# Optimization experiments

Measured on AMD Instinct MI355X. Metric: run time of the kernel, lower is better.

Reference implementation:

```python
import jax, jax.numpy as jnp
import numpy as np

B, C_IN, M = 512, 200, 128  # M = n_nodes + 1 (zero-pad slot 0)
N3 = 3 * (M - 1)            # 3 gather indices (node,left,right) per node
H1, H2, F = 512, 512, 256   # conv channel sizes, F = feature_dim


def tree_conv(data, idx, w, b):
    # data: [B, C, M]; idx: [B, 3N] int indices into M; w: [O, C, 3]; b: [O]
    gathered = jnp.take_along_axis(data, idx[:, None, :].astype(jnp.int32), axis=2)  # [B, C, 3N]
    g = gathered.reshape(data.shape[0], data.shape[1], -1, 3)  # [B, C, N, 3]
    out = jnp.einsum('bcnk,ock->bon', g, w) + b[None, :, None]  # Conv1d(k=3, stride=3)
    zero = jnp.zeros((data.shape[0], w.shape[0], 1), out.dtype)  # re-attach pad slot 0
    return jnp.concatenate([zero, out], axis=2)  # [B, O, M]


def tree_layer_norm(data):
    # per-tree normalization over (channel, node) dims; torch.std is unbiased (ddof=1)
    mean = jnp.mean(data, axis=(1, 2), keepdims=True)
    std = jnp.std(data, axis=(1, 2), keepdims=True, ddof=1)
    return (data - mean) / (std + 1e-5)


def setup_inputs() -> dict:
    key = jax.random.key(0)
    ks = jax.random.split(key, 16)
    s = 0.05
    inp = {
        'trees': jax.random.normal(ks[0], (B, C_IN, M), jnp.float32),
        'indexes': jax.random.randint(ks[1], (B, N3, 1), 0, M, jnp.int32),
        # plan_embedding_nn conv stack
        'w1': jax.random.normal(ks[2], (H1, C_IN, 3), jnp.float32) * s,
        'b1': jnp.zeros((H1,), jnp.float32),
        'w2': jax.random.normal(ks[3], (H2, H1, 3), jnp.float32) * s,
        'b2': jnp.zeros((H2,), jnp.float32),
        'w3': jax.random.normal(ks[4], (F, H2, 3), jnp.float32) * s,
        'b3': jnp.zeros((F,), jnp.float32),
        # gate_nn: Linear(F, F//2) ReLU Linear(F//2, 1)
        'gw1': jax.random.normal(ks[5], (F // 2, F), jnp.float32) * s,
        'gb1': jnp.zeros((F // 2,), jnp.float32),
        'gw2': jax.random.normal(ks[6], (1, F // 2), jnp.float32) * s,
        'gb2': jnp.zeros((1,), jnp.float32),
        'rw1': jax.random.normal(ks[7], (128, 2 * F), jnp.float32) * s,
        'rb1': jnp.zeros((128,), jnp.float32),
        'rw2': jax.random.normal(ks[8], (64, 128), jnp.float32) * s,
        'rb2': jnp.zeros((64,), jnp.float32),
        'rw3': jax.random.normal(ks[9], (1, 64), jnp.float32) * s,
        'rb3': jnp.zeros((1,), jnp.float32),
    }
    return inp


def reference(trees, indexes, w1, b1, w2, b2, w3, b3, gw1, gb1, gw2, gb2,
              rw1, rb1, rw2, rb2, rw3, rb3):
    idx = indexes[..., 0]  # [B, 3N]
    x = jax.nn.relu(tree_layer_norm(tree_conv(trees, idx, w1, b1)))
    x = jax.nn.relu(tree_layer_norm(tree_conv(x, idx, w2, b2)))
    emb = tree_conv(x, idx, w3, b3)            # [B, F, M]
    et = jnp.transpose(emb, (0, 2, 1))         # [B, M, F]
    # GlobalAttention pooling: segments are the equal-size per-plan node sets,
    # so segment-softmax == softmax over the node axis.
    gate = jax.nn.relu(jnp.einsum('bmf,hf->bmh', et, gw1) + gb1)
    gate = jnp.einsum('bmh,oh->bmo', gate, gw2) + gb2   # [B, M, 1]
    attn = jax.nn.softmax(gate, axis=1)
    pool = jnp.sum(attn * et, axis=1)          # [B, F]
    root = et[:, 1, :]                         # slot 1 = root node
    combined = jnp.concatenate([root, pool], axis=1)  # [B, 2F]
    h = jax.nn.relu(combined @ rw1.T + rb1)
    h = jax.nn.relu(h @ rw2.T + rb2)
    out = h @ rw3.T + rb3                      # [B, 1]
    return out, combined
```

## Files before the change

### kernel.cpp

```cpp
#include <hip/hip_runtime.h>
#include <stdint.h>

#define DI __device__ __forceinline__

static constexpr int B_   = 512;
static constexpr int N3_  = 381;

typedef short bf16x8 __attribute__((ext_vector_type(8)));
typedef float f32x4  __attribute__((ext_vector_type(4)));

DI float bf2f(uint32_t u) { union { uint32_t i; float f; } v; v.i = u << 16; return v.f; }
DI uint16_t f2bf(float f) {
  union { float f; uint32_t i; } v; v.f = f;
  uint32_t x = v.i;
  return (uint16_t)((x + 0x7fffu + ((x >> 16) & 1u)) >> 16);
}
DI void unpack8(uint4 u, float* v) {
  v[0] = bf2f(u.x & 0xffffu); v[1] = bf2f(u.x >> 16);
  v[2] = bf2f(u.y & 0xffffu); v[3] = bf2f(u.y >> 16);
  v[4] = bf2f(u.z & 0xffffu); v[5] = bf2f(u.z >> 16);
  v[6] = bf2f(u.w & 0xffffu); v[7] = bf2f(u.w >> 16);
}

DI void ldsload16(const uint16_t* g, uint16_t* l) {
  __builtin_amdgcn_global_load_lds((const __attribute__((address_space(1))) void*)g,
                                   (__attribute__((address_space(3))) void*)l,
                                   16, 0, 0);
}

__global__ void probe_kernel(const uint16_t* __restrict__ trees, int* __restrict__ flag,
                             float* __restrict__ statsAcc) {
  __shared__ int cnt;
  if (threadIdx.x == 0) cnt = 0;
  __syncthreads();
  int local = 0;
  #pragma unroll
  for (int q = 0; q < 2; q++) {
    uint16_t u = trees[threadIdx.x * 2 + q];
    int ex = (u >> 7) & 0xff;
    if (ex >= 110 && ex <= 133) local++;
  }
  atomicAdd(&cnt, local);
  #pragma unroll
  for (int q = 0; q < 8; q++) statsAcc[q * 256 + threadIdx.x] = 0.f;
  __syncthreads();
  if (threadIdx.x == 0) *flag = (cnt >= 450) ? 0 : 1;
}

__global__ void cvt_to_bf16(const void* __restrict__ src, uint16_t* __restrict__ dst,
                            int n, const int* __restrict__ flag) {
  int isf32 = *flag;
  int stride = gridDim.x * blockDim.x;
  for (int i = blockIdx.x * blockDim.x + threadIdx.x; i < n; i += stride)
    dst[i] = isf32 ? f2bf(((const float*)src)[i]) : ((const uint16_t*)src)[i];
}

__global__ void wcvt_kernel(const void* __restrict__ src, uint16_t* __restrict__ dst,
                            int O, int C, int Cpad, const int* __restrict__ flag) {
  int isf32 = *flag;
  int Kpad = 3 * Cpad;
  int n = O * Kpad;
  int stride = gridDim.x * blockDim.x;
  for (int i = blockIdx.x * blockDim.x + threadIdx.x; i < n; i += stride) {
    int o = i / Kpad, e = i - o * Kpad;
    int reg = e / Cpad, c = e - reg * Cpad;
    uint16_t v = 0;
    if (c < C) {
      int s = (o * C + c) * 3 + reg;
      v = isf32 ? f2bf(((const float*)src)[s]) : ((const uint16_t*)src)[s];
    }
    dst[i] = v;
  }
}

struct CvtJob { const void* src; float* dst; int n; };
struct CvtJobs { CvtJob j[13]; };
__global__ void cvt_many(CvtJobs jobs, int nj, const int* __restrict__ flag) {
  int isf32 = *flag;
  int stride = gridDim.x * blockDim.x;
  for (int k = 0; k < nj; k++) {
    const void* src = jobs.j[k].src;
    float* dst = jobs.j[k].dst;
    int n = jobs.j[k].n;
    for (int i = blockIdx.x * blockDim.x + threadIdx.x; i < n; i += stride)
      dst[i] = isf32 ? ((const float*)src)[i] : bf2f(((const uint16_t*)src)[i]);
  }
}

__global__ __launch_bounds__(256)
void transpose_trees(const void* __restrict__ trees, uint16_t* __restrict__ dst,
                     const int* __restrict__ flag) {
  __shared__ uint16_t sX[32][130];
  const int b = blockIdx.y, c0 = blockIdx.x * 32, tx = threadIdx.x;
  const int cn = min(32, 200 - c0);
  const int isf32 = *flag;

  if (isf32) {
    const float* src = (const float*)trees + ((size_t)b * 200 + c0) * 128;
    for (int t = tx; t < cn * 128; t += 256) {
      int c = t >> 7, m = t & 127;
      sX[c][m] = f2bf(src[c * 128 + m]);
    }
  } else {
    const uint32_t* src = (const uint32_t*)((const uint16_t*)trees + ((size_t)b * 200 + c0) * 128);
    for (int t = tx; t < cn * 64; t += 256) {
      int c = t >> 6, p = t & 63;
      ((uint32_t*)&sX[c][0])[p] = src[c * 64 + p];
    }
  }
  __syncthreads();

  uint32_t* out = (uint32_t*)(dst + (size_t)b * 129 * 256 + c0);
  for (int p = tx; p < 129 * 16; p += 256) {
    int m = p >> 4, u = p & 15;
    int c = u * 2;
    uint32_t v = 0;
    if (m < 128) {
      uint16_t lo = (c     < cn) ? sX[c][m]     : (uint16_t)0;
      uint16_t hi = (c + 1 < cn) ? sX[c + 1][m] : (uint16_t)0;
      v = (uint32_t)lo | ((uint32_t)hi << 16);
    }
    out[(size_t)m * 128 + u] = v;
  }
}

__global__ __launch_bounds__(256, 3)
void gemm_kernel(const uint16_t* __restrict__ A,
                 const uint16_t* __restrict__ xT,
                 const int* __restrict__ idxg,
                 const float* __restrict__ bias,
                 uint16_t* __restrict__ Y,
                 int nO, int Cpad, int outRS,
                 float* __restrict__ statsAcc) {
  __shared__ __align__(16) uint16_t sA[128 * 64];
  __shared__ __align__(16) uint16_t sB[128 * 64];
  __shared__ float sBias[128];
  __shared__ int sIdx[384];
  __shared__ float2 sRed[256];

  const int id   = blockIdx.x;
  const int xcd  = id & 7;
  const int rest = id >> 3;
  const int ot   = rest % nO;
  const int b    = (rest / nO) * 8 + xcd;
  const int obase = ot * 128;
  const int O     = nO * 128;

  const int tx    = threadIdx.x;
  const int wave  = tx >> 6, lane = tx & 63;
  const int wj    = wave & 1, wo = wave >> 1;
  const int Kpad  = 3 * Cpad;

  for (int t = tx; t < N3_; t += 256) sIdx[t] = idxg[(size_t)b * N3_ + t];
  if (tx < 128) sBias[tx] = bias[obase + tx];
  __syncthreads();

  const uint16_t* Abase = A + (size_t)obase * Kpad;
  const uint16_t* Bbase = xT + (size_t)b * 129 * Cpad;

  const int srow = lane >> 3;
  const int schk = lane & 7;
  const int lm = lane & 15;
  const int kg = lane >> 4;

  f32x4 zero4 = {0.f, 0.f, 0.f, 0.f};
  f32x4 acc[4][4];
  #pragma unroll
  for (int i = 0; i < 4; i++)
    #pragma unroll
    for (int j = 0; j < 4; j++) acc[i][j] = zero4;

  for (int reg = 0; reg < 3; reg++) {
    int ridx[4];
    #pragma unroll
    for (int i = 0; i < 4; i++) {
      int r = wave * 8 + i * 32 + srow;
      ridx[i] = (r == 0) ? 128 : sIdx[3 * (r - 1) + reg];
    }
    for (int co = 0; co < Cpad; co += 64) {
      __syncthreads();
      #pragma unroll
      for (int i = 0; i < 4; i++) {
        int r  = wave * 8 + i * 32 + srow;
        int ca = schk ^ (r & 7);
        ldsload16(Abase + (size_t)r * Kpad + reg * Cpad + co + ca * 8,
                  &sA[(wave * 8 + i * 32) * 64]);
        ldsload16(Bbase + (size_t)ridx[i] * Cpad + co + ca * 8,
                  &sB[(wave * 8 + i * 32) * 64]);
      }
      __syncthreads();
      #pragma unroll
      for (int s = 0; s < 2; s++) {
        bf16x8 xv[4], wv[4];
        #pragma unroll
        for (int f = 0; f < 4; f++) {
          int rj = wj * 64 + f * 16 + lm;
          int cj = (s * 4 + kg) ^ (rj & 7);
          xv[f] = *(const bf16x8*)&sB[rj * 64 + cj * 8];
          int ro = wo * 64 + f * 16 + lm;
          int cw = (s * 4 + kg) ^ (ro & 7);
          wv[f] = *(const bf16x8*)&sA[ro * 64 + cw * 8];
        }
        #pragma unroll
        for (int fj = 0; fj < 4; fj++)
          #pragma unroll
          for (int fo = 0; fo < 4; fo++)
            acc[fj][fo] = __builtin_amdgcn_mfma_f32_16x16x32_bf16(xv[fj], wv[fo], acc[fj][fo], 0, 0, 0);
      }
    }
  }

  float s1 = 0.f, s2 = 0.f;
  #pragma unroll
  for (int fj = 0; fj < 4; fj++) {
    #pragma unroll
    for (int fo = 0; fo < 4; fo++) {
      int olocal = wo * 64 + fo * 16 + lm;
      float bo = sBias[olocal];
      #pragma unroll
      for (int r = 0; r < 4; r++) {
        int j = wj * 64 + fj * 16 + kg * 4 + r;
        float v = acc[fj][fo][r] + bo;
        if (j == 0) v = 0.f;
        s1 += v; s2 += v * v;
        Y[((size_t)b * outRS + j) * O + obase + olocal] = f2bf(v);
      }
    }
  }

  if (statsAcc) {
    sRed[tx] = make_float2(s1, s2);
    __syncthreads();
    for (int s = 128; s > 0; s >>= 1) {
      if (tx < s) { sRed[tx].x += sRed[tx + s].x; sRed[tx].y += sRed[tx + s].y; }
      __syncthreads();
    }
    if (tx == 0) {
      atomicAdd(&statsAcc[b * 2],     sRed[0].x);
      atomicAdd(&statsAcc[b * 2 + 1], sRed[0].y);
    }
  }
}

__global__ void stats_finalize(const float* __restrict__ acc, float* __restrict__ ms,
                               int count, int nb) {
  int b = blockIdx.x * blockDim.x + threadIdx.x;
  if (b < nb) {
    float s = acc[b * 2], ss = acc[b * 2 + 1];
    float n = (float)count;
    float mean = s / n;
    float var = (ss - s * s / n) / (n - 1.0f);
    var = fmaxf(var, 0.f);
    ms[b * 2] = mean;
    ms[b * 2 + 1] = 1.0f / (sqrtf(var) + 1e-5f);
  }
}

__global__ __launch_bounds__(256)
void ln_relu_kernel(uint16_t* __restrict__ y, const float* __restrict__ ms) {
  const int total = B_ * 129 * 64;
  int stride = gridDim.x * blockDim.x;
  for (int i = blockIdx.x * blockDim.x + threadIdx.x; i < total; i += stride) {
    int rowG = i >> 6;
    int b = rowG / 129;
    int r = rowG - b * 129;
    uint4 out;
    if (r == 128) {
      out = make_uint4(0, 0, 0, 0);
    } else {
      float mean = ms[b * 2], scale = ms[b * 2 + 1];
      uint4 u = ((const uint4*)y)[i];
      float v[8]; unpack8(u, v);
      uint32_t rr[4];
      #pragma unroll
      for (int k = 0; k < 4; k++) {
        float a  = fmaxf((v[2 * k]     - mean) * scale, 0.f);
        float bb = fmaxf((v[2 * k + 1] - mean) * scale, 0.f);
        rr[k] = (uint32_t)f2bf(a) | ((uint32_t)f2bf(bb) << 16);
      }
      out = make_uint4(rr[0], rr[1], rr[2], rr[3]);
    }
    ((uint4*)y)[i] = out;
  }
}

__global__ __launch_bounds__(256)
void gate_kernel(const uint16_t* __restrict__ emb,
                 const uint16_t* __restrict__ gw1b,
                 const float* __restrict__ gb1,
                 const float* __restrict__ gw2, const float* __restrict__ gb2,
                 const float* __restrict__ rw1, const float* __restrict__ rb1,
                 const float* __restrict__ rw2, const float* __restrict__ rb2,
                 const float* __restrict__ rw3, const float* __restrict__ rb3,
                 void* __restrict__ dout, const int* __restrict__ flag) {
  __shared__ __align__(16) uint16_t sEmb[128 * 64];
  __shared__ float sRed[4][128];
  __shared__ float sSm[128];
  __shared__ float sAttn[128];
  __shared__ float sPool4[4 * 256];
  __shared__ __align__(16) float sC[512];
  __shared__ __align__(16) float sH1[128];
  __shared__ float sH2[64];

  const int b = blockIdx.x;
  const int tx = threadIdx.x;
  const int wave = tx >> 6, lane = tx & 63;
  const int lm = lane & 15, kg = lane >> 4;
  const int srow = lane >> 3, schk = lane & 7;
  const int h0 = wave * 32;
  const uint16_t* embB = emb + (size_t)b * 128 * 256;

  f32x4 zero4 = {0.f, 0.f, 0.f, 0.f};
  f32x4 acc[2][8];
  #pragma unroll
  for (int i = 0; i < 2; i++)
    #pragma unroll
    for (int t = 0; t < 8; t++) acc[i][t] = zero4;

  for (int kc = 0; kc < 256; kc += 64) {
    __syncthreads();
    #pragma unroll
    for (int i = 0; i < 4; i++) {
      int r  = wave * 8 + i * 32 + srow;
      int ca = schk ^ (r & 7);
      ldsload16(embB + (size_t)r * 256 + kc + ca * 8, &sEmb[(wave * 8 + i * 32) * 64]);
    }
    __syncthreads();
    #pragma unroll
    for (int s = 0; s < 2; s++) {
      bf16x8 a0 = *(const bf16x8*)(gw1b + (size_t)(h0 + lm) * 256 + kc + s * 32 + kg * 8);
      bf16x8 a1 = *(const bf16x8*)(gw1b + (size_t)(h0 + 16 + lm) * 256 + kc + s * 32 + kg * 8);
      #pragma unroll
      for (int t = 0; t < 8; t++) {
        int rn = t * 16 + lm;
        int cn = (s * 4 + kg) ^ (rn & 7);
        bf16x8 bv = *(const bf16x8*)&sEmb[rn * 64 + cn * 8];
        acc[0][t] = __builtin_amdgcn_mfma_f32_16x16x32_bf16(a0, bv, acc[0][t], 0, 0, 0);
        acc[1][t] = __builtin_amdgcn_mfma_f32_16x16x32_bf16(a1, bv, acc[1][t], 0, 0, 0);
      }
    }
  }

  float gb[2][4], gv[2][4];
  #pragma unroll
  for (int ht = 0; ht < 2; ht++)
    #pragma unroll
    for (int r = 0; r < 4; r++) {
      int h = h0 + ht * 16 + kg * 4 + r;
      gb[ht][r] = gb1[h]; gv[ht][r] = gw2[h];
    }
  float p[8];
  #pragma unroll
  for (int t = 0; t < 8; t++) {
    float s = 0.f;
    #pragma unroll
    for (int ht = 0; ht < 2; ht++)
      #pragma unroll
      for (int r = 0; r < 4; r++)
        s += fmaxf(acc[ht][t][r] + gb[ht][r], 0.f) * gv[ht][r];
    s += __shfl_xor(s, 16);
    s += __shfl_xor(s, 32);
    p[t] = s;
  }
  if (lane < 16) {
    #pragma unroll
    for (int t = 0; t < 8; t++) sRed[wave][t * 16 + lane] = p[t];
  }
  __syncthreads();

  float e = 0.f;
  if (tx < 128) {
    float v = sRed[0][tx] + sRed[1][tx] + sRed[2][tx] + sRed[3][tx] + gb2[0];
    sSm[tx] = v;
    sAttn[tx] = v;
  }
  __syncthreads();
  for (int s = 64; s > 0; s >>= 1) {
    if (tx < s) sSm[tx] = fmaxf(sSm[tx], sSm[tx + s]);
    __syncthreads();
  }
  float mx = sSm[0];
  __syncthreads();
  if (tx < 128) { e = expf(sAttn[tx] - mx); sSm[tx] = e; }
  __syncthreads();
  for (int s = 64; s > 0; s >>= 1) {
    if (tx < s) sSm[tx] += sSm[tx + s];
    __syncthreads();
  }
  float denom = sSm[0];
  __syncthreads();
  if (tx < 128) sAttn[tx] = e / denom;
  __syncthreads();

  float pl00 = 0.f, pl01 = 0.f, pl10 = 0.f, pl11 = 0.f;
  const uint32_t* base = (const uint32_t*)embB;
  const int mw = wave * 32;
  for (int mi = 0; mi < 32; mi++) {
    float a = sAttn[mw + mi];
    uint32_t u0 = base[(size_t)(mw + mi) * 128 + lane];
    uint32_t u1 = base[(size_t)(mw + mi) * 128 + 64 + lane];
    pl00 = fmaf(a, bf2f(u0 & 0xffffu), pl00);
    pl01 = fmaf(a, bf2f(u0 >> 16),     pl01);
    pl10 = fmaf(a, bf2f(u1 & 0xffffu), pl10);
    pl11 = fmaf(a, bf2f(u1 >> 16),     pl11);
  }
  sPool4[wave * 256 + lane * 2]           = pl00;
  sPool4[wave * 256 + lane * 2 + 1]       = pl01;
  sPool4[wave * 256 + 128 + lane * 2]     = pl10;
  sPool4[wave * 256 + 128 + lane * 2 + 1] = pl11;
  __syncthreads();

  float pool = sPool4[tx] + sPool4[256 + tx] + sPool4[512 + tx] + sPool4[768 + tx];
  float root = bf2f(embB[256 + tx]);
  sC[tx]       = root;
  sC[256 + tx] = pool;

  const int isf32 = (*flag != 0);
  if (!isf32) {
    uint16_t* o = ((uint16_t*)dout) + 512;
    o[b * 512 + tx]       = f2bf(root);
    o[b * 512 + 256 + tx] = f2bf(pool);
  } else {
    float* o = ((float*)dout) + 512;
    o[b * 512 + tx]       = root;
    o[b * 512 + 256 + tx] = pool;
  }
  __syncthreads();

  if (tx < 128) {
    float a = rb1[tx];
    const float4* wr = (const float4*)(rw1 + (size_t)tx * 512);
    for (int i = 0; i < 128; i++) {
      float4 w4 = wr[i];
      float4 c4 = *(const float4*)&sC[i * 4];
      a = fmaf(w4.x, c4.x, a); a = fmaf(w4.y, c4.y, a);
      a = fmaf(w4.z, c4.z, a); a = fmaf(w4.w, c4.w, a);
    }
    sH1[tx] = fmaxf(a, 0.f);
  }
  __syncthreads();
  if (tx < 64) {
    float a2 = rb2[tx];
    const float4* wr2 = (const float4*)(rw2 + (size_t)tx * 128);
    for (int i = 0; i < 32; i++) {
      float4 w4 = wr2[i];
      float4 h4 = *(const float4*)&sH1[i * 4];
      a2 = fmaf(w4.x, h4.x, a2); a2 = fmaf(w4.y, h4.y, a2);
      a2 = fmaf(w4.z, h4.z, a2); a2 = fmaf(w4.w, h4.w, a2);
    }
    sH2[tx] = fmaxf(a2, 0.f);
  }
  __syncthreads();
  if (tx < 64) {
    float pv = sH2[tx] * rw3[tx];
    for (int off = 32; off > 0; off >>= 1) pv += __shfl_down(pv, off);
    if (tx == 0) {
      float o = pv + rb3[0];
      if (!isf32) ((uint16_t*)dout)[b] = f2bf(o);
      else        ((float*)dout)[b]    = o;
    }
  }
}

extern "C" void kernel_launch(void* const* d_in, const int* in_sizes, int n_in,
                              void* d_out, int out_size, void* d_ws, size_t ws_size,
                              hipStream_t stream) {
  const void* trees   = d_in[0];
  const int*  indexes = (const int*)d_in[1];
  const void* w1 = d_in[2];  const void* b1 = d_in[3];
  const void* w2 = d_in[4];  const void* b2 = d_in[5];
  const void* w3 = d_in[6];  const void* b3 = d_in[7];
  const void* gw1 = d_in[8]; const void* gb1 = d_in[9];
  const void* gw2 = d_in[10]; const void* gb2 = d_in[11];
  const void* rw1 = d_in[12]; const void* rb1 = d_in[13];
  const void* rw2 = d_in[14]; const void* rb2 = d_in[15];
  const void* rw3 = d_in[16]; const void* rb3 = d_in[17];

  char* ws = (char*)d_ws;
  size_t off = 0;
  auto alloc = [&](size_t bytes) -> char* {
    char* p = ws + off;
    off += (bytes + 255) & ~(size_t)255;
    return p;
  };

  int*   flagp    = (int*)alloc(256);
  float* statsAcc = (float*)alloc(4 * B_ * sizeof(float));
  float* statsMS  = (float*)alloc(4 * B_ * sizeof(float));
  float* b1f = (float*)alloc(512 * 4);
  float* b2f = (float*)alloc(512 * 4);
  float* b3f = (float*)alloc(256 * 4);
  float* gb1f = (float*)alloc(128 * 4);
  float* gw2f = (float*)alloc(128 * 4);
  float* gb2f = (float*)alloc(4);
  float* rw1f = (float*)alloc(128 * 512 * 4);
  float* rb1f = (float*)alloc(128 * 4);
  float* rw2f = (float*)alloc(64 * 128 * 4);
  float* rb2f = (float*)alloc(64 * 4);
  float* rw3f = (float*)alloc(64 * 4);
  float* rb3f = (float*)alloc(4);
  uint16_t* W1b  = (uint16_t*)alloc((size_t)512 * 768 * 2);
  uint16_t* W2b  = (uint16_t*)alloc((size_t)512 * 1536 * 2);
  uint16_t* W3b  = (uint16_t*)alloc((size_t)256 * 1536 * 2);
  uint16_t* GW1b = (uint16_t*)alloc((size_t)128 * 256 * 2);
  uint16_t* bufA = (uint16_t*)alloc((size_t)B_ * 129 * 512 * 2);
  uint16_t* bufB = (uint16_t*)alloc((size_t)B_ * 129 * 512 * 2);

  uint16_t* treesT = bufB;
  uint16_t* y1T    = bufA;
  uint16_t* y2T    = bufB;
  uint16_t* yT3    = bufA;

  probe_kernel<<<1, 256, 0, stream>>>((const uint16_t*)trees, flagp, statsAcc);
  transpose_trees<<<dim3(7, B_), 256, 0, stream>>>(trees, treesT, flagp);
  wcvt_kernel<<<1024, 256, 0, stream>>>(w1, W1b, 512, 200, 256, flagp);
  wcvt_kernel<<<2048, 256, 0, stream>>>(w2, W2b, 512, 512, 512, flagp);
  wcvt_kernel<<<1024, 256, 0, stream>>>(w3, W3b, 256, 512, 512, flagp);
  cvt_to_bf16<<<256, 256, 0, stream>>>(gw1, GW1b, 128 * 256, flagp);

  CvtJobs jobs;
  int ji = 0;
  auto addjob = [&](const void* s, float* d, int n) { jobs.j[ji].src = s; jobs.j[ji].dst = d; jobs.j[ji].n = n; ji++; };
  addjob(b1, b1f, 512); addjob(b2, b2f, 512); addjob(b3, b3f, 256);
  addjob(gb1, gb1f, 128);
  addjob(gw2, gw2f, 128);       addjob(gb2, gb2f, 1);
  addjob(rw1, rw1f, 128 * 512); addjob(rb1, rb1f, 128);
  addjob(rw2, rw2f, 64 * 128);  addjob(rb2, rb2f, 64);
  addjob(rw3, rw3f, 64);        addjob(rb3, rb3f, 1);
  cvt_many<<<256, 256, 0, stream>>>(jobs, ji, flagp);

  gemm_kernel<<<4 * B_, 256, 0, stream>>>(
      W1b, treesT, indexes, b1f, y1T, 4, 256, 129, statsAcc);
  stats_finalize<<<2, 256, 0, stream>>>(statsAcc, statsMS, 512 * 128, B_);
  ln_relu_kernel<<<2048, 256, 0, stream>>>(y1T, statsMS);

  gemm_kernel<<<4 * B_, 256, 0, stream>>>(
      W2b, y1T, indexes, b2f, y2T, 4, 512, 129, statsAcc + 2 * B_);
  stats_finalize<<<2, 256, 0, stream>>>(statsAcc + 2 * B_, statsMS + 2 * B_, 512 * 128, B_);
  ln_relu_kernel<<<2048, 256, 0, stream>>>(y2T, statsMS + 2 * B_);

  gemm_kernel<<<2 * B_, 256, 0, stream>>>(
      W3b, y2T, indexes, b3f, yT3, 2, 512, 128, nullptr);

  gate_kernel<<<B_, 256, 0, stream>>>(yT3, GW1b, gb1f, gw2f, gb2f,
                                      rw1f, rb1f, rw2f, rb2f, rw3f, rb3f,
                                      d_out, flagp);

  (void)in_sizes; (void)n_in; (void)out_size; (void)ws_size;
}
```

Baseline: 465.5 us.

## Merge preprocessing kernels into one launch and fold stats finalize into LN

Replaces the probe, transpose, weight-convert and small-parameter convert kernels with a single prep kernel that partitions its blocks by job, with every block recomputing the dtype probe locally. Removes the two stats_finalize launches by computing mean and inverse std inline in ln_relu_kernel. Also raises gemm_kernel launch bounds occupancy hint from 3 to 4. The aim is to cut launch count and inter-kernel gaps, at the cost of redundant probe work per block and possible register pressure in the GEMM.

```diff
diff --git a/kernel.cpp b/kernel.cpp
--- a/kernel.cpp
+++ b/kernel.cpp
@@ -28,40 +28,31 @@
                                    16, 0, 0);
 }
 
-__global__ void probe_kernel(const uint16_t* __restrict__ trees, int* __restrict__ flag,
-                             float* __restrict__ statsAcc) {
-  __shared__ int cnt;
-  if (threadIdx.x == 0) cnt = 0;
-  __syncthreads();
-  int local = 0;
-  #pragma unroll
-  for (int q = 0; q < 2; q++) {
-    uint16_t u = trees[threadIdx.x * 2 + q];
-    int ex = (u >> 7) & 0xff;
-    if (ex >= 110 && ex <= 133) local++;
-  }
-  atomicAdd(&cnt, local);
-  #pragma unroll
-  for (int q = 0; q < 8; q++) statsAcc[q * 256 + threadIdx.x] = 0.f;
-  __syncthreads();
-  if (threadIdx.x == 0) *flag = (cnt >= 450) ? 0 : 1;
-}
-
-__global__ void cvt_to_bf16(const void* __restrict__ src, uint16_t* __restrict__ dst,
-                            int n, const int* __restrict__ flag) {
-  int isf32 = *flag;
-  int stride = gridDim.x * blockDim.x;
-  for (int i = blockIdx.x * blockDim.x + threadIdx.x; i < n; i += stride)
-    dst[i] = isf32 ? f2bf(((const float*)src)[i]) : ((const uint16_t*)src)[i];
-}
-
-__global__ void wcvt_kernel(const void* __restrict__ src, uint16_t* __restrict__ dst,
-                            int O, int C, int Cpad, const int* __restrict__ flag) {
-  int isf32 = *flag;
+struct PrepArgs {
+  const void* trees; const void* w1; const void* w2; const void* w3; const void* gw1;
+  const void* b1; const void* b2; const void* b3; const void* gb1;
+  const void* gw2; const void* gb2;
+  const void* rw1; const void* rb1; const void* rw2; const void* rb2;
+  const void* rw3; const void* rb3;
+  uint16_t* treesT; uint16_t* W1b; uint16_t* W2b; uint16_t* W3b; uint16_t* GW1b;
+  float* b1f; float* b2f; float* b3f; float* gb1f; float* gw2f; float* gb2f;
+  float* rw1f; float* rb1f; float* rw2f; float* rb2f; float* rw3f; float* rb3f;
+  int* flagp; float* statsAcc;
+};
+
+static constexpr int PREP_TRANS_END = 3584;
+static constexpr int PREP_W1_END    = 3840;
+static constexpr int PREP_W2_END    = 4352;
+static constexpr int PREP_W3_END    = 4608;
+static constexpr int PREP_GW1_END   = 4640;
+static constexpr int PREP_F32_END   = 4672;
+  
+DI void wcvt_range(const void* src, uint16_t* dst, int O, int C, int Cpad,
+                   int isf32, int idx, int nb) {
   int Kpad = 3 * Cpad;
   int n = O * Kpad;
-  int stride = gridDim.x * blockDim.x;
-  for (int i = blockIdx.x * blockDim.x + threadIdx.x; i < n; i += stride) {
+  int stride = nb * 256;
+  for (int i = idx * 256 + (int)threadIdx.x; i < n; i += stride) {
     int o = i / Kpad, e = i - o * Kpad;
     int reg = e / Cpad, c = e - reg * Cpad;
     uint16_t v = 0;
@@ -73,58 +64,102 @@
   }
 }
 
-struct CvtJob { const void* src; float* dst; int n; };
-struct CvtJobs { CvtJob j[13]; };
-__global__ void cvt_many(CvtJobs jobs, int nj, const int* __restrict__ flag) {
-  int isf32 = *flag;
-  int stride = gridDim.x * blockDim.x;
-  for (int k = 0; k < nj; k++) {
-    const void* src = jobs.j[k].src;
-    float* dst = jobs.j[k].dst;
-    int n = jobs.j[k].n;
-    for (int i = blockIdx.x * blockDim.x + threadIdx.x; i < n; i += stride)
-      dst[i] = isf32 ? ((const float*)src)[i] : bf2f(((const uint16_t*)src)[i]);
-  }
+DI void fcvt_range(const void* src, float* dst, int n, int isf32, int idx, int nb) {
+  int stride = nb * 256;
+  for (int i = idx * 256 + (int)threadIdx.x; i < n; i += stride)
+    dst[i] = isf32 ? ((const float*)src)[i] : bf2f(((const uint16_t*)src)[i]);
 }
 
 __global__ __launch_bounds__(256)
-void transpose_trees(const void* __restrict__ trees, uint16_t* __restrict__ dst,
-                     const int* __restrict__ flag) {
+void prep_kernel(PrepArgs a) {
+  __shared__ int cnt;
   __shared__ uint16_t sX[32][130];
-  const int b = blockIdx.y, c0 = blockIdx.x * 32, tx = threadIdx.x;
-  const int cn = min(32, 200 - c0);
-  const int isf32 = *flag;
-
-  if (isf32) {
-    const float* src = (const float*)trees + ((size_t)b * 200 + c0) * 128;
-    for (int t = tx; t < cn * 128; t += 256) {
-      int c = t >> 7, m = t & 127;
-      sX[c][m] = f2bf(src[c * 128 + m]);
-    }
+
+  const int id = blockIdx.x;
+  const int tx = threadIdx.x;
+
+  if (tx == 0) cnt = 0;
+  __syncthreads();
+  {
+    const uint16_t* t16 = (const uint16_t*)a.trees;
+    int local = 0;
+    #pragma unroll
+    for (int q = 0; q < 2; q++) {
+      uint16_t u = t16[tx * 2 + q];
+      int ex = (u >> 7) & 0xff;
+      if (ex >= 110 && ex <= 133) local++;
+    }
+    atomicAdd(&cnt, local);
+  }
+  __syncthreads();
+  const int isf32 = (cnt >= 450) ? 0 : 1;
+
+  if (id == 0) {
+    if (tx == 0) *a.flagp = isf32;
+    #pragma unroll
+    for (int q = 0; q < 8; q++) a.statsAcc[q * 256 + tx] = 0.f;
+  }
+
+  if (id < PREP_TRANS_END) {
+    const int b = id / 7, c0 = (id % 7) * 32;
+    const int cn = min(32, 200 - c0);
+    if (isf32) {
+      const float* src = (const float*)a.trees + ((size_t)b * 200 + c0) * 128;
+      for (int t = tx; t < cn * 128; t += 256) {
+        int c = t >> 7, m = t & 127;
+        sX[c][m] = f2bf(src[c * 128 + m]);
+      }
+    } else {
+      const uint32_t* src = (const uint32_t*)((const uint16_t*)a.trees + ((size_t)b * 200 + c0) * 128);
+      for (int t = tx; t < cn * 64; t += 256) {
+        int c = t >> 6, p = t & 63;
+        ((uint32_t*)&sX[c][0])[p] = src[c * 64 + p];
+      }
+    }
+    __syncthreads();
+    uint32_t* out = (uint32_t*)(a.treesT + (size_t)b * 129 * 256 + c0);
+    for (int p = tx; p < 129 * 16; p += 256) {
+      int m = p >> 4, u = p & 15;
+      int c = u * 2;
+      uint32_t v = 0;
+      if (m < 128) {
+        uint16_t lo = (c     < cn) ? sX[c][m]     : (uint16_t)0;
+        uint16_t hi = (c + 1 < cn) ? sX[c + 1][m] : (uint16_t)0;
+        v = (uint32_t)lo | ((uint32_t)hi << 16);
+      }
+      out[(size_t)m * 128 + u] = v;
+    }
+  } else if (id < PREP_W1_END) {
+    wcvt_range(a.w1, a.W1b, 512, 200, 256, isf32, id - PREP_TRANS_END, PREP_W1_END - PREP_TRANS_END);
+  } else if (id < PREP_W2_END) {
+    wcvt_range(a.w2, a.W2b, 512, 512, 512, isf32, id - PREP_W1_END, PREP_W2_END - PREP_W1_END);
+  } else if (id < PREP_W3_END) {
+    wcvt_range(a.w3, a.W3b, 256, 512, 512, isf32, id - PREP_W2_END, PREP_W3_END - PREP_W2_END);
+  } else if (id < PREP_GW1_END) {
+    int idx = id - PREP_W3_END, nb = PREP_GW1_END - PREP_W3_END;
+    int stride = nb * 256;
+    for (int i = idx * 256 + tx; i < 128 * 256; i += stride)
+      a.GW1b[i] = isf32 ? f2bf(((const float*)a.gw1)[i]) : ((const uint16_t*)a.gw1)[i];
   } else {
-    const uint32_t* src = (const uint32_t*)((const uint16_t*)trees + ((size_t)b * 200 + c0) * 128);
-    for (int t = tx; t < cn * 64; t += 256) {
-      int c = t >> 6, p = t & 63;
-      ((uint32_t*)&sX[c][0])[p] = src[c * 64 + p];
-    }
-  }
-  __syncthreads();
-
-  uint32_t* out = (uint32_t*)(dst + (size_t)b * 129 * 256 + c0);
-  for (int p = tx; p < 129 * 16; p += 256) {
-    int m = p >> 4, u = p & 15;
-    int c = u * 2;
-    uint32_t v = 0;
-    if (m < 128) {
-      uint16_t lo = (c     < cn) ? sX[c][m]     : (uint16_t)0;
-      uint16_t hi = (c + 1 < cn) ? sX[c + 1][m] : (uint16_t)0;
-      v = (uint32_t)lo | ((uint32_t)hi << 16);
-    }
-    out[(size_t)m * 128 + u] = v;
-  }
-}
-
-__global__ __launch_bounds__(256, 3)
+    int idx = id - PREP_GW1_END, nb = PREP_F32_END - PREP_GW1_END;
+    fcvt_range(a.rw1, a.rw1f, 128 * 512, isf32, idx, nb);
+    fcvt_range(a.rw2, a.rw2f, 64 * 128, isf32, idx, nb);
+    if (idx == 0) {
+      fcvt_range(a.b1, a.b1f, 512, isf32, 0, 1);
+      fcvt_range(a.b2, a.b2f, 512, isf32, 0, 1);
+      fcvt_range(a.b3, a.b3f, 256, isf32, 0, 1);
+      fcvt_range(a.gb1, a.gb1f, 128, isf32, 0, 1);
+      fcvt_range(a.gw2, a.gw2f, 128, isf32, 0, 1);
+      fcvt_range(a.gb2, a.gb2f, 1, isf32, 0, 1);
+      fcvt_range(a.rb1, a.rb1f, 128, isf32, 0, 1);
+      fcvt_range(a.rb2, a.rb2f, 64, isf32, 0, 1);
+      fcvt_range(a.rw3, a.rw3f, 64, isf32, 0, 1);
+      fcvt_range(a.rb3, a.rb3f, 1, isf32, 0, 1);
+    }
+  }
+}
+
+__global__ __launch_bounds__(256, 4)
 void gemm_kernel(const uint16_t* __restrict__ A,
                  const uint16_t* __restrict__ xT,
                  const int* __restrict__ idxg,
@@ -242,22 +277,9 @@
   }
 }
 
-__global__ void stats_finalize(const float* __restrict__ acc, float* __restrict__ ms,
-                               int count, int nb) {
-  int b = blockIdx.x * blockDim.x + threadIdx.x;
-  if (b < nb) {
-    float s = acc[b * 2], ss = acc[b * 2 + 1];
-    float n = (float)count;
-    float mean = s / n;
-    float var = (ss - s * s / n) / (n - 1.0f);
-    var = fmaxf(var, 0.f);
-    ms[b * 2] = mean;
-    ms[b * 2 + 1] = 1.0f / (sqrtf(var) + 1e-5f);
-  }
-}
-
 __global__ __launch_bounds__(256)
-void ln_relu_kernel(uint16_t* __restrict__ y, const float* __restrict__ ms) {
+void ln_relu_kernel(uint16_t* __restrict__ y, const float* __restrict__ statsAcc,
+                    float count) {
   const int total = B_ * 129 * 64;
   int stride = gridDim.x * blockDim.x;
   for (int i = blockIdx.x * blockDim.x + threadIdx.x; i < total; i += stride) {
@@ -268,7 +290,10 @@
     if (r == 128) {
       out = make_uint4(0, 0, 0, 0);
     } else {
-      float mean = ms[b * 2], scale = ms[b * 2 + 1];
+      float s = statsAcc[b * 2], ss = statsAcc[b * 2 + 1];
+      float mean = s / count;
+      float var = fmaxf((ss - s * s / count) / (count - 1.0f), 0.f);
+      float scale = 1.0f / (sqrtf(var) + 1e-5f);
       uint4 u = ((const uint4*)y)[i];
       float v[8]; unpack8(u, v);
       uint32_t rr[4];
@@ -467,14 +492,6 @@
                               hipStream_t stream) {
   const void* trees   = d_in[0];
   const int*  indexes = (const int*)d_in[1];
-  const void* w1 = d_in[2];  const void* b1 = d_in[3];
-  const void* w2 = d_in[4];  const void* b2 = d_in[5];
-  const void* w3 = d_in[6];  const void* b3 = d_in[7];
-  const void* gw1 = d_in[8]; const void* gb1 = d_in[9];
-  const void* gw2 = d_in[10]; const void* gb2 = d_in[11];
-  const void* rw1 = d_in[12]; const void* rb1 = d_in[13];
-  const void* rw2 = d_in[14]; const void* rb2 = d_in[15];
-  const void* rw3 = d_in[16]; const void* rb3 = d_in[17];
 
   char* ws = (char*)d_ws;
   size_t off = 0;
@@ -486,7 +503,6 @@
 
   int*   flagp    = (int*)alloc(256);
   float* statsAcc = (float*)alloc(4 * B_ * sizeof(float));
-  float* statsMS  = (float*)alloc(4 * B_ * sizeof(float));
   float* b1f = (float*)alloc(512 * 4);
   float* b2f = (float*)alloc(512 * 4);
   float* b3f = (float*)alloc(256 * 4);
@@ -511,33 +527,30 @@
   uint16_t* y2T    = bufB;
   uint16_t* yT3    = bufA;
 
-  probe_kernel<<<1, 256, 0, stream>>>((const uint16_t*)trees, flagp, statsAcc);
-  transpose_trees<<<dim3(7, B_), 256, 0, stream>>>(trees, treesT, flagp);
-  wcvt_kernel<<<1024, 256, 0, stream>>>(w1, W1b, 512, 200, 256, flagp);
-  wcvt_kernel<<<2048, 256, 0, stream>>>(w2, W2b, 512, 512, 512, flagp);
-  wcvt_kernel<<<1024, 256, 0, stream>>>(w3, W3b, 256, 512, 512, flagp);
-  cvt_to_bf16<<<256, 256, 0, stream>>>(gw1, GW1b, 128 * 256, flagp);
-
-  CvtJobs jobs;
-  int ji = 0;
-  auto addjob = [&](const void* s, float* d, int n) { jobs.j[ji].src = s; jobs.j[ji].dst = d; jobs.j[ji].n = n; ji++; };
-  addjob(b1, b1f, 512); addjob(b2, b2f, 512); addjob(b3, b3f, 256);
-  addjob(gb1, gb1f, 128);
-  addjob(gw2, gw2f, 128);       addjob(gb2, gb2f, 1);
-  addjob(rw1, rw1f, 128 * 512); addjob(rb1, rb1f, 128);
-  addjob(rw2, rw2f, 64 * 128);  addjob(rb2, rb2f, 64);
-  addjob(rw3, rw3f, 64);        addjob(rb3, rb3f, 1);
-  cvt_many<<<256, 256, 0, stream>>>(jobs, ji, flagp);
+  PrepArgs pa;
+  pa.trees = trees;
+  pa.w1 = d_in[2];  pa.b1 = d_in[3];
+  pa.w2 = d_in[4];  pa.b2 = d_in[5];
+  pa.w3 = d_in[6];  pa.b3 = d_in[7];
+  pa.gw1 = d_in[8]; pa.gb1 = d_in[9];
+  pa.gw2 = d_in[10]; pa.gb2 = d_in[11];
+  pa.rw1 = d_in[12]; pa.rb1 = d_in[13];
+  pa.rw2 = d_in[14]; pa.rb2 = d_in[15];
+  pa.rw3 = d_in[16]; pa.rb3 = d_in[17];
+  pa.treesT = treesT; pa.W1b = W1b; pa.W2b = W2b; pa.W3b = W3b; pa.GW1b = GW1b;
+  pa.b1f = b1f; pa.b2f = b2f; pa.b3f = b3f; pa.gb1f = gb1f; pa.gw2f = gw2f; pa.gb2f = gb2f;
+  pa.rw1f = rw1f; pa.rb1f = rb1f; pa.rw2f = rw2f; pa.rb2f = rb2f; pa.rw3f = rw3f; pa.rb3f = rb3f;
+  pa.flagp = flagp; pa.statsAcc = statsAcc;
+
+  prep_kernel<<<PREP_F32_END, 256, 0, stream>>>(pa);
 
   gemm_kernel<<<4 * B_, 256, 0, stream>>>(
       W1b, treesT, indexes, b1f, y1T, 4, 256, 129, statsAcc);
-  stats_finalize<<<2, 256, 0, stream>>>(statsAcc, statsMS, 512 * 128, B_);
-  ln_relu_kernel<<<2048, 256, 0, stream>>>(y1T, statsMS);
+  ln_relu_kernel<<<2048, 256, 0, stream>>>(y1T, statsAcc, 65536.f);
 
   gemm_kernel<<<4 * B_, 256, 0, stream>>>(
       W2b, y1T, indexes, b2f, y2T, 4, 512, 129, statsAcc + 2 * B_);
-  stats_finalize<<<2, 256, 0, stream>>>(statsAcc + 2 * B_, statsMS + 2 * B_, 512 * 128, B_);
-  ln_relu_kernel<<<2048, 256, 0, stream>>>(y2T, statsMS + 2 * B_);
+  ln_relu_kernel<<<2048, 256, 0, stream>>>(y2T, statsAcc + 2 * B_, 65536.f);
 
   gemm_kernel<<<2 * B_, 256, 0, stream>>>(
       W3b, y2T, indexes, b3f, yT3, 2, 512, 128, nullptr);
```

New measurement: 429.3 us. 1.08x faster.
